# Performance work log

Measured on AMD Instinct MI355X. Metric: run time of the kernel, lower is better.

The kernel has to match this reference:

```python
import jax, jax.numpy as jnp
import numpy as np

RATIO = (0.25, 0.25)  # init arg: fraction of low frequencies to zero out


def dct_matrix(n):
    """Orthonormal DCT-II matrix D such that D @ v = dct(v, norm='ortho')."""
    k = jnp.arange(n, dtype=jnp.float32)[:, None]
    i = jnp.arange(n, dtype=jnp.float32)[None, :]
    m = jnp.cos(jnp.pi * (2.0 * i + 1.0) * k / (2.0 * n)) * jnp.sqrt(2.0 / n)
    m = m.at[0].multiply(1.0 / jnp.sqrt(2.0))
    return m  # [n, n]


def setup_inputs() -> dict:
    key = jax.random.key(0)
    x = jax.random.normal(key, (16, 96, 224, 224), dtype=jnp.float32)
    return {"x": x}


def reference(x):
    b, c, h, w = x.shape
    Dh = dct_matrix(h)  # [h, h]
    Dw = dct_matrix(w)  # [w, w]

    # high-pass mask: zero out low-frequency top-left block
    h0 = int(h * RATIO[0])
    w0 = int(w * RATIO[1])
    mask = jnp.ones((h, w), dtype=x.dtype)
    mask = mask.at[:h0, :w0].set(0.0)

    # 2D DCT (separable): F = Dh @ x @ Dw^T over last two dims
    f = jnp.einsum('hi,bciw->bchw', Dh, x)
    f = jnp.einsum('bchj,wj->bchw', f, Dw)

    f = f * mask  # broadcast [h,w] over [b,c,h,w]

    # 2D IDCT (inverse of orthonormal transform = transpose): Dh^T @ F @ Dw
    g = jnp.einsum('ih,bchw->bciw', Dh, f)
    g = jnp.einsum('bciw,jw->bcij', g, Dw)

    return x * g
```

## Files before the change

kernel.cpp:

```cpp
#include <hip/hip_runtime.h>
#include <hip/hip_bf16.h>

#define H    224
#define HW   50176
#define KCUT 56
#define JH   112
#define LDSRS 464
#define LDSB (JH * LDSRS)
#define LDS_BYTES (2 * LDSB)

#define OFF_D  0
#define OFF_M  50176
#define OFF_P  (OFF_M + 25088)

#define DPI 3.14159265358979323846

typedef __attribute__((ext_vector_type(8))) short short8;
typedef __attribute__((ext_vector_type(4))) float f32x4;

__device__ __forceinline__ f32x4 mfma_bf16(short8 a, short8 b, f32x4 c) {
    return __builtin_amdgcn_mfma_f32_16x16x32_bf16(a, b, c, 0, 0, 0);
}

__device__ __forceinline__ short bf16b(float f) {
    __hip_bfloat16 h = __float2bfloat16(f);
    return *reinterpret_cast<short*>(&h);
}

__device__ __forceinline__ short8 cvt8(const float* p) {
    const float4 v0 = *(const float4*)p;
    const float4 v1 = *(const float4*)(p + 4);
    short8 r;
    r[0] = bf16b(v0.x); r[1] = bf16b(v0.y); r[2] = bf16b(v0.z); r[3] = bf16b(v0.w);
    r[4] = bf16b(v1.x); r[5] = bf16b(v1.y); r[6] = bf16b(v1.z); r[7] = bf16b(v1.w);
    return r;
}

__global__ void k_build_D(float* __restrict__ D) {
    int idx = blockIdx.x * 256 + threadIdx.x;
    if (idx >= HW) return;
    int k = idx / H, i = idx - k * H;
    double v = cos(DPI * (2.0 * i + 1.0) * (double)k / (2.0 * H)) * sqrt(2.0 / H);
    if (k == 0) v *= 0.70710678118654752440;
    D[idx] = (float)v;
}

__global__ void k_build_MP(const float* __restrict__ D,
                           __hip_bfloat16* __restrict__ Mb,
                           __hip_bfloat16* __restrict__ Pb) {
    int idx = blockIdx.x * 256 + threadIdx.x;
    if (idx >= HW) return;
    int i = idx / H, j = idx - i * H;
    float m = 0.f, p = 0.f;
    for (int k = 0; k < H; ++k) {
        float t = D[i * H + k] * D[k * H + j];
        m += t;
        if (k < KCUT) p += t;
    }
    Mb[idx] = __float2bfloat16(m);
    Pb[idx] = __float2bfloat16(p);
}

__global__ __launch_bounds__(448, 2)
void k_fused(const float* __restrict__ X,
             const __hip_bfloat16* __restrict__ Mb,
             const __hip_bfloat16* __restrict__ Pb,
             float* __restrict__ Out)
{
    extern __shared__ __align__(16) char lds[];

    const int Bid = blockIdx.x;
    const int xcd = Bid & 7, ix = Bid >> 3;
    const int p   = xcd * 192 + (ix >> 1);
    const int j0b = (ix & 1) * JH;
    const float* x  = X   + (size_t)p * HW;
    float*      out = Out + (size_t)p * HW;

    const int t = threadIdx.x;
    const int w = t >> 6, l = t & 63;
    const int col = l & 15, q = l >> 4;
    const int koff = q * 8;

    f32x4 acc[2][14];
    #pragma unroll
    for (int i = 0; i < 2; ++i)
        #pragma unroll
        for (int j = 0; j < 14; ++j) acc[i][j] = (f32x4)0.f;

    const float* xa0 = x + (size_t)(32 * w + col) * H + koff;
    const float* xa1 = xa0 + 16 * H;
    const __hip_bfloat16* Mj = Mb + (size_t)(j0b + col) * H + koff;
    const __hip_bfloat16* Pj = Pb + (size_t)(j0b + col) * H + koff;

    #pragma unroll 1
    for (int ks = 0; ks < 7; ++ks) {
        const int k0 = ks * 32;
        const short8 a0 = cvt8(xa0 + k0);
        const short8 a1 = cvt8(xa1 + k0);
        #pragma unroll
        for (int nt = 0; nt < 7; ++nt) {
            const short8 b = *(const short8*)(Mj + nt * 16 * H + k0);
            acc[0][nt] = mfma_bf16(a0, b, acc[0][nt]);
            acc[1][nt] = mfma_bf16(a1, b, acc[1][nt]);
        }
        #pragma unroll
        for (int nt = 0; nt < 7; ++nt) {
            const short8 b = *(const short8*)(Pj + nt * 16 * H + k0);
            acc[0][7 + nt] = mfma_bf16(a0, b, acc[0][7 + nt]);
            acc[1][7 + nt] = mfma_bf16(a1, b, acc[1][7 + nt]);
        }
    }

    #pragma unroll
    for (int im = 0; im < 2; ++im) {
        const int kk2 = (32 * w + 16 * im + 4 * q) * 2;
        #pragma unroll
        for (int nt = 0; nt < 14; ++nt) {
            const int jj   = (nt < 7 ? nt : nt - 7) * 16 + col;
            const int base = (nt < 7 ? 0 : LDSB);
            const float sgn = (nt < 7 ? 1.f : -1.f);
            short t4[4];
            #pragma unroll
            for (int r = 0; r < 4; ++r) t4[r] = bf16b(sgn * acc[im][nt][r]);
            *(uint2*)(lds + base + jj * LDSRS + kk2) = *(uint2*)t4;
        }
    }

    __syncthreads();

    f32x4 o[14];
    #pragma unroll
    for (int j = 0; j < 14; ++j) o[j] = (f32x4)0.f;

    const int jj = 16 * w + col;
    const __hip_bfloat16* Mi = Mb + (size_t)col * H + koff;
    const __hip_bfloat16* Pi = Pb + (size_t)col * H + koff;

    #pragma unroll 1
    for (int ks = 0; ks < 7; ++ks) {
        const int k0 = ks * 32;
        const short8 a = *(const short8*)(lds + jj * LDSRS + (k0 + koff) * 2);
        #pragma unroll
        for (int it = 0; it < 14; ++it) {
            const short8 b = *(const short8*)(Mi + it * 16 * H + k0);
            o[it] = mfma_bf16(a, b, o[it]);
        }
    }
    #pragma unroll 1
    for (int ks = 0; ks < 7; ++ks) {
        const int k0 = ks * 32;
        const short8 a = *(const short8*)(lds + LDSB + jj * LDSRS + (k0 + koff) * 2);
        #pragma unroll
        for (int it = 0; it < 14; ++it) {
            const short8 b = *(const short8*)(Pi + it * 16 * H + k0);
            o[it] = mfma_bf16(a, b, o[it]);
        }
    }

    const int jw = j0b + 16 * w + 4 * q;
    #pragma unroll
    for (int it = 0; it < 14; ++it) {
        const int i = it * 16 + col;
        const size_t off = (size_t)i * H + jw;
        const float4 xv = *(const float4*)(x + off);
        float4 ov;
        ov.x = xv.x * o[it][0];
        ov.y = xv.y * o[it][1];
        ov.z = xv.z * o[it][2];
        ov.w = xv.w * o[it][3];
        *(float4*)(out + off) = ov;
    }
}

extern "C" void kernel_launch(void* const* d_in, const int* in_sizes, int n_in,
                              void* d_out, int out_size, void* d_ws, size_t ws_size,
                              hipStream_t stream) {
    const float* x = (const float*)d_in[0];
    float* out = (float*)d_out;
    float* w = (float*)d_ws;
    float* D = w + OFF_D;
    __hip_bfloat16* Mb = (__hip_bfloat16*)(w + OFF_M);
    __hip_bfloat16* Pb = (__hip_bfloat16*)(w + OFF_P);

    k_build_D <<<dim3((HW + 255) / 256), dim3(256), 0, stream>>>(D);
    k_build_MP<<<dim3((HW + 255) / 256), dim3(256), 0, stream>>>(D, Mb, Pb);
    k_fused   <<<dim3(3072), dim3(448), LDS_BYTES, stream>>>(x, Mb, Pb, out);
}
```

Measured before the change: 1.152 ms.

## Double block threads to 896 and halve per-warp tiles in fused DCT kernel

The fused kernel now runs 14 waves per block instead of 7. In stage one each wave computes a single 16-row tile, and in stage two each wave covers half of the output rows, so each wave keeps half as many accumulators. The aim is more waves in flight to hide global-memory latency, and lower register pressure, without changing total MFMA work. The setup kernel that builds M and P is also restructured: it computes the partial sum over the first KCUT terms with 8-way split accumulators and reuses those sums for the full sum, which changes the summation order slightly. Each wave now reuses its A fragments less and issues more B loads per MFMA, and launch_bounds(896,4) may force register spills.

After: 1.090 ms. 1.06x faster.

```diff
diff --git a/kernel.cpp b/kernel.cpp
--- a/kernel.cpp
+++ b/kernel.cpp
@@ -51,17 +51,36 @@
     int idx = blockIdx.x * 256 + threadIdx.x;
     if (idx >= HW) return;
     int i = idx / H, j = idx - i * H;
-    float m = 0.f, p = 0.f;
-    for (int k = 0; k < H; ++k) {
-        float t = D[i * H + k] * D[k * H + j];
-        m += t;
-        if (k < KCUT) p += t;
-    }
+    const float* Di = D + (size_t)i * H;
+    const float* Dj = D + j;
+    float s0=0.f,s1=0.f,s2=0.f,s3=0.f,s4=0.f,s5=0.f,s6=0.f,s7=0.f;
+    for (int k = 0; k < KCUT; k += 8) {
+        s0 += Di[k+0] * Dj[(size_t)(k+0)*H];
+        s1 += Di[k+1] * Dj[(size_t)(k+1)*H];
+        s2 += Di[k+2] * Dj[(size_t)(k+2)*H];
+        s3 += Di[k+3] * Dj[(size_t)(k+3)*H];
+        s4 += Di[k+4] * Dj[(size_t)(k+4)*H];
+        s5 += Di[k+5] * Dj[(size_t)(k+5)*H];
+        s6 += Di[k+6] * Dj[(size_t)(k+6)*H];
+        s7 += Di[k+7] * Dj[(size_t)(k+7)*H];
+    }
+    const float p = ((s0+s1)+(s2+s3)) + ((s4+s5)+(s6+s7));
+    for (int k = KCUT; k < H; k += 8) {
+        s0 += Di[k+0] * Dj[(size_t)(k+0)*H];
+        s1 += Di[k+1] * Dj[(size_t)(k+1)*H];
+        s2 += Di[k+2] * Dj[(size_t)(k+2)*H];
+        s3 += Di[k+3] * Dj[(size_t)(k+3)*H];
+        s4 += Di[k+4] * Dj[(size_t)(k+4)*H];
+        s5 += Di[k+5] * Dj[(size_t)(k+5)*H];
+        s6 += Di[k+6] * Dj[(size_t)(k+6)*H];
+        s7 += Di[k+7] * Dj[(size_t)(k+7)*H];
+    }
+    const float m = ((s0+s1)+(s2+s3)) + ((s4+s5)+(s6+s7));
     Mb[idx] = __float2bfloat16(m);
     Pb[idx] = __float2bfloat16(p);
 }
 
-__global__ __launch_bounds__(448, 2)
+__global__ __launch_bounds__(896, 4)
 void k_fused(const float* __restrict__ X,
              const __hip_bfloat16* __restrict__ Mb,
              const __hip_bfloat16* __restrict__ Pb,
@@ -81,39 +100,32 @@
     const int col = l & 15, q = l >> 4;
     const int koff = q * 8;
 
-    f32x4 acc[2][14];
+    f32x4 acc[14];
     #pragma unroll
-    for (int i = 0; i < 2; ++i)
-        #pragma unroll
-        for (int j = 0; j < 14; ++j) acc[i][j] = (f32x4)0.f;
-
-    const float* xa0 = x + (size_t)(32 * w + col) * H + koff;
-    const float* xa1 = xa0 + 16 * H;
+    for (int j = 0; j < 14; ++j) acc[j] = (f32x4)0.f;
+
+    const float* xa = x + (size_t)(16 * w + col) * H + koff;
     const __hip_bfloat16* Mj = Mb + (size_t)(j0b + col) * H + koff;
     const __hip_bfloat16* Pj = Pb + (size_t)(j0b + col) * H + koff;
 
     #pragma unroll 1
     for (int ks = 0; ks < 7; ++ks) {
         const int k0 = ks * 32;
-        const short8 a0 = cvt8(xa0 + k0);
-        const short8 a1 = cvt8(xa1 + k0);
+        const short8 a = cvt8(xa + k0);
         #pragma unroll
         for (int nt = 0; nt < 7; ++nt) {
             const short8 b = *(const short8*)(Mj + nt * 16 * H + k0);
-            acc[0][nt] = mfma_bf16(a0, b, acc[0][nt]);
-            acc[1][nt] = mfma_bf16(a1, b, acc[1][nt]);
+            acc[nt] = mfma_bf16(a, b, acc[nt]);
         }
         #pragma unroll
         for (int nt = 0; nt < 7; ++nt) {
             const short8 b = *(const short8*)(Pj + nt * 16 * H + k0);
-            acc[0][7 + nt] = mfma_bf16(a0, b, acc[0][7 + nt]);
-            acc[1][7 + nt] = mfma_bf16(a1, b, acc[1][7 + nt]);
-        }
-    }
-
-    #pragma unroll
-    for (int im = 0; im < 2; ++im) {
-        const int kk2 = (32 * w + 16 * im + 4 * q) * 2;
+            acc[7 + nt] = mfma_bf16(a, b, acc[7 + nt]);
+        }
+    }
+
+    {
+        const int kk2 = (16 * w + 4 * q) * 2;
         #pragma unroll
         for (int nt = 0; nt < 14; ++nt) {
             const int jj   = (nt < 7 ? nt : nt - 7) * 16 + col;
@@ -121,27 +133,28 @@
             const float sgn = (nt < 7 ? 1.f : -1.f);
             short t4[4];
             #pragma unroll
-            for (int r = 0; r < 4; ++r) t4[r] = bf16b(sgn * acc[im][nt][r]);
+            for (int r = 0; r < 4; ++r) t4[r] = bf16b(sgn * acc[nt][r]);
             *(uint2*)(lds + base + jj * LDSRS + kk2) = *(uint2*)t4;
         }
     }
 
     __syncthreads();
 
-    f32x4 o[14];
+    f32x4 o[7];
     #pragma unroll
-    for (int j = 0; j < 14; ++j) o[j] = (f32x4)0.f;
-
-    const int jj = 16 * w + col;
-    const __hip_bfloat16* Mi = Mb + (size_t)col * H + koff;
-    const __hip_bfloat16* Pi = Pb + (size_t)col * H + koff;
+    for (int j = 0; j < 7; ++j) o[j] = (f32x4)0.f;
+
+    const int jt = w >> 1, ih = w & 1;
+    const int jj = 16 * jt + col;
+    const __hip_bfloat16* Mi = Mb + (size_t)(ih * JH + col) * H + koff;
+    const __hip_bfloat16* Pi = Pb + (size_t)(ih * JH + col) * H + koff;
 
     #pragma unroll 1
     for (int ks = 0; ks < 7; ++ks) {
         const int k0 = ks * 32;
         const short8 a = *(const short8*)(lds + jj * LDSRS + (k0 + koff) * 2);
         #pragma unroll
-        for (int it = 0; it < 14; ++it) {
+        for (int it = 0; it < 7; ++it) {
             const short8 b = *(const short8*)(Mi + it * 16 * H + k0);
             o[it] = mfma_bf16(a, b, o[it]);
         }
@@ -151,16 +164,16 @@
         const int k0 = ks * 32;
         const short8 a = *(const short8*)(lds + LDSB + jj * LDSRS + (k0 + koff) * 2);
         #pragma unroll
-        for (int it = 0; it < 14; ++it) {
+        for (int it = 0; it < 7; ++it) {
             const short8 b = *(const short8*)(Pi + it * 16 * H + k0);
             o[it] = mfma_bf16(a, b, o[it]);
         }
     }
 
-    const int jw = j0b + 16 * w + 4 * q;
+    const int jw = j0b + 16 * jt + 4 * q;
     #pragma unroll
-    for (int it = 0; it < 14; ++it) {
-        const int i = it * 16 + col;
+    for (int it = 0; it < 7; ++it) {
+        const int i = ih * JH + it * 16 + col;
         const size_t off = (size_t)i * H + jw;
         const float4 xv = *(const float4*)(x + off);
         float4 ov;
@@ -184,5 +197,5 @@
 
     k_build_D <<<dim3((HW + 255) / 256), dim3(256), 0, stream>>>(D);
     k_build_MP<<<dim3((HW + 255) / 256), dim3(256), 0, stream>>>(D, Mb, Pb);
-    k_fused   <<<dim3(3072), dim3(448), LDS_BYTES, stream>>>(x, Mb, Pb, out);
-}
+    k_fused   <<<dim3(3072), dim3(896), LDS_BYTES, stream>>>(x, Mb, Pb, out);
+}
```
